# Performance work log

Measured on AMD Instinct MI355X. Metric: run time of the kernel, lower is better.

The kernel has to match this reference:

```python
import jax, jax.numpy as jnp
import numpy as np

N_NODES = 100000
N_EDGES = 3200000  # avg degree 32
D_IN = 256
D_OUT = 256


def setup_inputs() -> dict:
    key = jax.random.key(0)
    k1, k2, k3, k4 = jax.random.split(key, 4)
    x = jax.random.normal(k1, (N_NODES, D_IN), dtype=jnp.float32)
    # nn.Linear(in, out, bias=False): weight shape [out, in]
    W = jax.random.normal(k2, (D_OUT, D_IN), dtype=jnp.float32) / np.sqrt(D_IN).astype(np.float32)
    bias = jnp.zeros((D_OUT,), dtype=jnp.float32)
    rows = jax.random.randint(k3, (N_EDGES,), 0, N_NODES, dtype=jnp.int32)
    cols = jax.random.randint(k4, (N_EDGES,), 0, N_NODES, dtype=jnp.int32)
    return {"x": x, "W": W, "bias": bias, "rows": rows, "cols": cols}


def reference(x, W, bias, rows, cols):
    # aggr == 'planetoid-gcn-residual' branch; dropout p=0 (identity).
    n = x.shape[0]
    h = x @ W.T + bias                                      # [N, D_out]
    # adj_t.sum(dim=-1): per-row degree of binary adjacency
    deg = jax.ops.segment_sum(jnp.ones(rows.shape, x.dtype), rows, num_segments=n)
    norm = jax.lax.rsqrt(1.0 + deg)[:, None]                # [N, 1]
    h = norm * h
    # spmm_add(adj_t, h)[i] = sum_{(i,j) in E} h[j]
    agg = jax.ops.segment_sum(h[cols], rows, num_segments=n)
    h = agg + h
    return norm * h
```

## Files before the change

kernel.cpp:

```cpp
#include <hip/hip_runtime.h>
#include <hip/hip_fp16.h>
#include <stdint.h>


#define THREADS 256

typedef _Float16 half8 __attribute__((ext_vector_type(8)));
typedef float floatx4 __attribute__((ext_vector_type(4)));

__global__ void rank_kernel(const int* __restrict__ rows, int* __restrict__ cnt,
                            int* __restrict__ rank, int E) {
    int e = (blockIdx.x * THREADS + threadIdx.x) * 4;
    if (e + 3 < E) {
        int4 r4 = *(const int4*)(rows + e);
        int4 k;
        k.x = atomicAdd(&cnt[r4.x], 1);
        k.y = atomicAdd(&cnt[r4.y], 1);
        k.z = atomicAdd(&cnt[r4.z], 1);
        k.w = atomicAdd(&cnt[r4.w], 1);
        *(int4*)(rank + e) = k;
    } else {
        for (int i = e; i < E && i < e + 4; ++i)
            rank[i] = atomicAdd(&cnt[rows[i]], 1);
    }
}

__global__ void scanA(const int* __restrict__ cnt, int* __restrict__ rs,
                      int* __restrict__ bsums, int n) {
    __shared__ int s[THREADS];
    int tid  = threadIdx.x;
    int base = blockIdx.x * 1024 + tid * 4;
    int v0 = (base + 0 < n) ? cnt[base + 0] : 0;
    int v1 = (base + 1 < n) ? cnt[base + 1] : 0;
    int v2 = (base + 2 < n) ? cnt[base + 2] : 0;
    int v3 = (base + 3 < n) ? cnt[base + 3] : 0;
    int sum = v0 + v1 + v2 + v3;
    s[tid] = sum;
    __syncthreads();
    for (int off = 1; off < THREADS; off <<= 1) {
        int t = (tid >= off) ? s[tid - off] : 0;
        __syncthreads();
        s[tid] += t;
        __syncthreads();
    }
    int run = s[tid] - sum;
    if (base + 0 < n) rs[base + 0] = run;  run += v0;
    if (base + 1 < n) rs[base + 1] = run;  run += v1;
    if (base + 2 < n) rs[base + 2] = run;  run += v2;
    if (base + 3 < n) rs[base + 3] = run;
    if (tid == THREADS - 1) bsums[blockIdx.x] = s[THREADS - 1];
}

__global__ void scanB(int* __restrict__ bsums, int nb) {
    __shared__ int s[THREADS];
    int tid = threadIdx.x;
    int v = (tid < nb) ? bsums[tid] : 0;
    s[tid] = v;
    __syncthreads();
    for (int off = 1; off < THREADS; off <<= 1) {
        int t = (tid >= off) ? s[tid - off] : 0;
        __syncthreads();
        s[tid] += t;
        __syncthreads();
    }
    if (tid < nb) bsums[tid] = s[tid] - v;
}

__global__ void scanC(int* __restrict__ rs, const int* __restrict__ bsums, int n, int E) {
    int tid  = threadIdx.x;
    int base = blockIdx.x * 1024 + tid * 4;
    int add  = bsums[blockIdx.x];
    if (base + 0 < n) rs[base + 0] += add;
    if (base + 1 < n) rs[base + 1] += add;
    if (base + 2 < n) rs[base + 2] += add;
    if (base + 3 < n) rs[base + 3] += add;
    if (blockIdx.x == 0 && tid == 0) rs[n] = E;
}

__global__ void scatter2(const int* __restrict__ rows, const int* __restrict__ cols,
                         const int* __restrict__ rank, const int* __restrict__ rs,
                         int* __restrict__ csr_col, int E) {
    int e = (blockIdx.x * THREADS + threadIdx.x) * 4;
    if (e + 3 < E) {
        int4 r4 = *(const int4*)(rows + e);
        int4 c4 = *(const int4*)(cols + e);
        int4 k4 = *(const int4*)(rank + e);
        csr_col[rs[r4.x] + k4.x] = c4.x;
        csr_col[rs[r4.y] + k4.y] = c4.y;
        csr_col[rs[r4.z] + k4.z] = c4.z;
        csr_col[rs[r4.w] + k4.w] = c4.w;
    } else {
        for (int i = e; i < E && i < e + 4; ++i)
            csr_col[rs[rows[i]] + rank[i]] = cols[i];
    }
}

__global__ void make_bswz(const float* __restrict__ W, half8* __restrict__ Bswz) {
    int t = blockIdx.x * THREADS + threadIdx.x;
    int n_tile = t >> 9;
    int k_step = (t >> 6) & 7;
    int lane   = t & 63;
    int q = lane >> 4, m16 = lane & 15;
    const float* src = W + (size_t)(n_tile * 16 + m16) * 256 + k_step * 32 + q * 8;
    half8 h;
#pragma unroll
    for (int j = 0; j < 8; j++) h[j] = (_Float16)src[j];
    Bswz[t] = h;
}

__device__ __forceinline__ int As_swz(int b) {
    return b ^ ((((b >> 10) & 7) ^ (((b >> 8) & 1) << 3)) << 4);
}

__global__ __launch_bounds__(THREADS) void gemm_mfma(
    const float* __restrict__ x, const half8* __restrict__ Bswz,
    const float* __restrict__ bias, const int* __restrict__ rs,
    _Float16* __restrict__ h16, int n) {
    __shared__ _Float16 As[4 * 8 * 64 * 8];
    int tid  = threadIdx.x;
    int row0 = blockIdx.x * 64;

#pragma unroll
    for (int i = 0; i < 16; i++) {
        int flat = i * THREADS + tid;
        int r  = flat >> 6;
        int k  = (flat & 63) * 4;
        float4 v;
        if (row0 + r < n) v = *(const float4*)(x + (size_t)(row0 + r) * 256 + k);
        else { v.x = 0.f; v.y = 0.f; v.z = 0.f; v.w = 0.f; }
        int m_sub  = r >> 4;
        int k_step = k >> 5;
        int q      = (k >> 3) & 3;
        int j      = k & 7;
        int lane_w = (r & 15) + (q << 4);
        int entry  = (m_sub * 8 + k_step) * 64 + lane_w;
        union { _Float16 h[4]; uint2 u; } pk;
        pk.h[0] = (_Float16)v.x; pk.h[1] = (_Float16)v.y;
        pk.h[2] = (_Float16)v.z; pk.h[3] = (_Float16)v.w;
        *(uint2*)((char*)As + As_swz(entry * 16 + (j << 1))) = pk.u;
    }
    __syncthreads();

    int w    = tid >> 6;
    int lane = tid & 63;

    floatx4 acc[4][4];
#pragma unroll
    for (int ms = 0; ms < 4; ms++)
#pragma unroll
        for (int nn = 0; nn < 4; nn++) {
            acc[ms][nn][0] = 0.f; acc[ms][nn][1] = 0.f;
            acc[ms][nn][2] = 0.f; acc[ms][nn][3] = 0.f;
        }

    for (int ks = 0; ks < 8; ks++) {
        half8 bfrag[4];
#pragma unroll
        for (int nn = 0; nn < 4; nn++)
            bfrag[nn] = Bswz[((w * 4 + nn) * 8 + ks) * 64 + lane];
        half8 afrag[4];
#pragma unroll
        for (int ms = 0; ms < 4; ms++)
            afrag[ms] = *(const half8*)((char*)As +
                            As_swz(((ms * 8 + ks) * 64 + lane) * 16));
#pragma unroll
        for (int ms = 0; ms < 4; ms++)
#pragma unroll
            for (int nn = 0; nn < 4; nn++)
                acc[ms][nn] = __builtin_amdgcn_mfma_f32_16x16x32_f16(
                    afrag[ms], bfrag[nn], acc[ms][nn], 0, 0, 0);
    }

    int rgrp = lane >> 4;
    int cl   = lane & 15;
#pragma unroll
    for (int ms = 0; ms < 4; ms++) {
        int rbase = row0 + ms * 16 + rgrp * 4;
        float nrm[4];
#pragma unroll
        for (int i = 0; i < 4; i++) {
            int r = rbase + i;
            nrm[i] = (r < n) ? rsqrtf(1.0f + (float)(rs[r + 1] - rs[r])) : 0.f;
        }
#pragma unroll
        for (int nn = 0; nn < 4; nn++) {
            int col = w * 64 + nn * 16 + cl;
            float bb = bias[col];
#pragma unroll
            for (int i = 0; i < 4; i++) {
                int r = rbase + i;
                if (r < n)
                    h16[(size_t)r * 256 + col] =
                        (_Float16)((acc[ms][nn][i] + bb) * nrm[i]);
            }
        }
    }
}

__global__ __launch_bounds__(THREADS) void agg_half(
    const _Float16* __restrict__ h16, const int* __restrict__ csr_col,
    const int* __restrict__ rs, float* __restrict__ out, int n, int halfsel) {
    int row = blockIdx.x * 4 + (threadIdx.x >> 6);
    if (row >= n) return;
    int lane = threadIdx.x & 63;
    int g    = lane >> 4;
    int l16  = lane & 15;
    int off  = halfsel * 128 + l16 * 8;
    const _Float16* hb = h16 + off;

    int s   = rs[row];
    int end = rs[row + 1];

    float acc[8] = {0.f, 0.f, 0.f, 0.f, 0.f, 0.f, 0.f, 0.f};
    if (g == 0) {
        half8 v = *(const half8*)(hb + (size_t)row * 256);
#pragma unroll
        for (int j = 0; j < 8; j++) acc[j] = (float)v[j];
    }

    int e = s + g;
    for (; e + 4 < end; e += 8) {
        int c0 = csr_col[e];
        int c1 = csr_col[e + 4];
        half8 v0 = *(const half8*)(hb + (size_t)c0 * 256);
        half8 v1 = *(const half8*)(hb + (size_t)c1 * 256);
#pragma unroll
        for (int j = 0; j < 8; j++) acc[j] += (float)v0[j] + (float)v1[j];
    }
    for (; e < end; e += 4) {
        int c = csr_col[e];
        half8 v = *(const half8*)(hb + (size_t)c * 256);
#pragma unroll
        for (int j = 0; j < 8; j++) acc[j] += (float)v[j];
    }

#pragma unroll
    for (int j = 0; j < 8; j++) acc[j] += __shfl_down(acc[j], 32);
#pragma unroll
    for (int j = 0; j < 8; j++) acc[j] += __shfl_down(acc[j], 16);

    if (g == 0) {
        float nrm = rsqrtf(1.0f + (float)(end - s));
        float4 o0, o1;
        o0.x = acc[0] * nrm; o0.y = acc[1] * nrm; o0.z = acc[2] * nrm; o0.w = acc[3] * nrm;
        o1.x = acc[4] * nrm; o1.y = acc[5] * nrm; o1.z = acc[6] * nrm; o1.w = acc[7] * nrm;
        float* dst = out + (size_t)row * 256 + off;
        *(float4*)dst       = o0;
        *(float4*)(dst + 4) = o1;
    }
}

extern "C" void kernel_launch(void* const* d_in, const int* in_sizes, int n_in,
                              void* d_out, int out_size, void* d_ws, size_t ws_size,
                              hipStream_t stream) {
    const float* x    = (const float*)d_in[0];
    const float* W    = (const float*)d_in[1];
    const float* bias = (const float*)d_in[2];
    const int*   rows = (const int*)d_in[3];
    const int*   cols = (const int*)d_in[4];

    const int D = 256;
    int n = in_sizes[0] / D;
    int E = in_sizes[3];

    char* p = (char*)d_ws;
    auto alignup = [](size_t v) { return (v + 255) & ~(size_t)255; };
    _Float16* h16 = (_Float16*)p; p += alignup((size_t)n * D * sizeof(_Float16));
    int*   cnt    = (int*)p;    p += alignup((size_t)n * sizeof(int));
    int*   rs     = (int*)p;    p += alignup((size_t)(n + 1) * sizeof(int));
    int*   bsums  = (int*)p;    p += alignup((size_t)1024);
    int*   csr    = (int*)p;    p += alignup((size_t)E * sizeof(int));
    half8* Bswz   = (half8*)p;  p += alignup((size_t)8192 * sizeof(half8));

    int* rank = (int*)h16;

    hipMemsetAsync(cnt, 0, (size_t)n * sizeof(int), stream);

    int e4blocks = ((E + 3) / 4 + THREADS - 1) / THREADS;
    rank_kernel<<<e4blocks, THREADS, 0, stream>>>(rows, cnt, rank, E);

    int nb = (n + 1023) / 1024;
    scanA<<<nb, THREADS, 0, stream>>>(cnt, rs, bsums, n);
    scanB<<<1, THREADS, 0, stream>>>(bsums, nb);
    scanC<<<nb, THREADS, 0, stream>>>(rs, bsums, n, E);

    scatter2<<<e4blocks, THREADS, 0, stream>>>(rows, cols, rank, rs, csr, E);

    make_bswz<<<32, THREADS, 0, stream>>>(W, Bswz);

    int gblocks = (n + 63) / 64;
    gemm_mfma<<<gblocks, THREADS, 0, stream>>>(x, Bswz, bias, rs, h16, n);

    int ablocks = (n + 3) / 4;
    agg_half<<<ablocks, THREADS, 0, stream>>>(h16, csr, rs, (float*)d_out, n, 0);
    agg_half<<<ablocks, THREADS, 0, stream>>>(h16, csr, rs, (float*)d_out, n, 1);
}
```

Before: 666.9 us.

## Build CSR via two-level bucket sort with shared-memory histograms

```diff
diff --git a/kernel.cpp b/kernel.cpp
--- a/kernel.cpp
+++ b/kernel.cpp
@@ -4,36 +4,46 @@
 
 
 #define THREADS 256
+#define MAXBUCK 800
+#define B3_EDGES 16384
 
 typedef _Float16 half8 __attribute__((ext_vector_type(8)));
 typedef float floatx4 __attribute__((ext_vector_type(4)));
 
-__global__ void rank_kernel(const int* __restrict__ rows, int* __restrict__ cnt,
-                            int* __restrict__ rank, int E) {
-    int e = (blockIdx.x * THREADS + threadIdx.x) * 4;
-    if (e + 3 < E) {
-        int4 r4 = *(const int4*)(rows + e);
-        int4 k;
-        k.x = atomicAdd(&cnt[r4.x], 1);
-        k.y = atomicAdd(&cnt[r4.y], 1);
-        k.z = atomicAdd(&cnt[r4.z], 1);
-        k.w = atomicAdd(&cnt[r4.w], 1);
-        *(int4*)(rank + e) = k;
-    } else {
-        for (int i = e; i < E && i < e + 4; ++i)
-            rank[i] = atomicAdd(&cnt[rows[i]], 1);
-    }
-}
-
-__global__ void scanA(const int* __restrict__ cnt, int* __restrict__ rs,
-                      int* __restrict__ bsums, int n) {
+__global__ __launch_bounds__(THREADS) void bucket_count(
+    const int* __restrict__ rows, int* __restrict__ bcnt, int E, int nbuck) {
+    __shared__ int h[MAXBUCK];
+    for (int b = threadIdx.x; b < nbuck; b += THREADS) h[b] = 0;
+    __syncthreads();
+    int nquad  = E >> 2;
+    int stride = gridDim.x * THREADS;
+    for (int q = blockIdx.x * THREADS + threadIdx.x; q < nquad; q += stride) {
+        int4 r = ((const int4*)rows)[q];
+        atomicAdd(&h[r.x >> 7], 1);
+        atomicAdd(&h[r.y >> 7], 1);
+        atomicAdd(&h[r.z >> 7], 1);
+        atomicAdd(&h[r.w >> 7], 1);
+    }
+    if (blockIdx.x == 0)
+        for (int e = (nquad << 2) + threadIdx.x; e < E; e += THREADS)
+            atomicAdd(&h[rows[e] >> 7], 1);
+    __syncthreads();
+    for (int b = threadIdx.x; b < nbuck; b += THREADS) {
+        int v = h[b];
+        if (v) atomicAdd(&bcnt[b], v);
+    }
+}
+
+__global__ __launch_bounds__(THREADS) void bucket_scan(
+    const int* __restrict__ bcnt, int* __restrict__ boff, int* __restrict__ bcur,
+    int nbuck, int E) {
     __shared__ int s[THREADS];
-    int tid  = threadIdx.x;
-    int base = blockIdx.x * 1024 + tid * 4;
-    int v0 = (base + 0 < n) ? cnt[base + 0] : 0;
-    int v1 = (base + 1 < n) ? cnt[base + 1] : 0;
-    int v2 = (base + 2 < n) ? cnt[base + 2] : 0;
-    int v3 = (base + 3 < n) ? cnt[base + 3] : 0;
+    int tid = threadIdx.x;
+    int i0  = tid * 4;
+    int v0 = (i0 + 0 < nbuck) ? bcnt[i0 + 0] : 0;
+    int v1 = (i0 + 1 < nbuck) ? bcnt[i0 + 1] : 0;
+    int v2 = (i0 + 2 < nbuck) ? bcnt[i0 + 2] : 0;
+    int v3 = (i0 + 3 < nbuck) ? bcnt[i0 + 3] : 0;
     int sum = v0 + v1 + v2 + v3;
     s[tid] = sum;
     __syncthreads();
@@ -44,54 +54,75 @@
         __syncthreads();
     }
     int run = s[tid] - sum;
-    if (base + 0 < n) rs[base + 0] = run;  run += v0;
-    if (base + 1 < n) rs[base + 1] = run;  run += v1;
-    if (base + 2 < n) rs[base + 2] = run;  run += v2;
-    if (base + 3 < n) rs[base + 3] = run;
-    if (tid == THREADS - 1) bsums[blockIdx.x] = s[THREADS - 1];
-}
-
-__global__ void scanB(int* __restrict__ bsums, int nb) {
-    __shared__ int s[THREADS];
-    int tid = threadIdx.x;
-    int v = (tid < nb) ? bsums[tid] : 0;
-    s[tid] = v;
-    __syncthreads();
-    for (int off = 1; off < THREADS; off <<= 1) {
-        int t = (tid >= off) ? s[tid - off] : 0;
+    if (i0 + 0 < nbuck) { boff[i0 + 0] = run; bcur[i0 + 0] = run; }  run += v0;
+    if (i0 + 1 < nbuck) { boff[i0 + 1] = run; bcur[i0 + 1] = run; }  run += v1;
+    if (i0 + 2 < nbuck) { boff[i0 + 2] = run; bcur[i0 + 2] = run; }  run += v2;
+    if (i0 + 3 < nbuck) { boff[i0 + 3] = run; bcur[i0 + 3] = run; }
+    if (tid == 0) boff[nbuck] = E;
+}
+
+__global__ __launch_bounds__(THREADS) void bucket_scatter(
+    const int* __restrict__ rows, const int* __restrict__ cols,
+    int* __restrict__ bcur, int2* __restrict__ buf, int E, int nbuck) {
+    __shared__ int h[MAXBUCK];
+    __shared__ int lbase[MAXBUCK];
+    for (int b = threadIdx.x; b < nbuck; b += THREADS) h[b] = 0;
+    __syncthreads();
+    int e0 = blockIdx.x * B3_EDGES;
+    int e1 = e0 + B3_EDGES; if (e1 > E) e1 = E;
+    for (int e = e0 + threadIdx.x; e < e1; e += THREADS)
+        atomicAdd(&h[rows[e] >> 7], 1);
+    __syncthreads();
+    for (int b = threadIdx.x; b < nbuck; b += THREADS) {
+        int v = h[b];
+        lbase[b] = v ? atomicAdd(&bcur[b], v) : 0;
+        h[b] = 0;
+    }
+    __syncthreads();
+    for (int e = e0 + threadIdx.x; e < e1; e += THREADS) {
+        int r = rows[e];
+        int c = cols[e];
+        int b = r >> 7;
+        int p = lbase[b] + atomicAdd(&h[b], 1);
+        buf[p] = make_int2(r, c);
+    }
+}
+
+__global__ __launch_bounds__(THREADS) void csr_finalize(
+    const int2* __restrict__ buf, const int* __restrict__ boff,
+    int* __restrict__ rs, int* __restrict__ csr, int n, int E) {
+    int b = blockIdx.x;
+    __shared__ int h[128];
+    __shared__ int base[128];
+    if (threadIdx.x < 128) h[threadIdx.x] = 0;
+    __syncthreads();
+    int s = boff[b], e = boff[b + 1];
+    for (int i = s + threadIdx.x; i < e; i += THREADS)
+        atomicAdd(&h[buf[i].x & 127], 1);
+    __syncthreads();
+    if (threadIdx.x < 128) base[threadIdx.x] = h[threadIdx.x];
+    __syncthreads();
+    for (int off = 1; off < 128; off <<= 1) {
+        int t = 0;
+        if (threadIdx.x < 128 && threadIdx.x >= off) t = base[threadIdx.x - off];
         __syncthreads();
-        s[tid] += t;
+        if (threadIdx.x < 128) base[threadIdx.x] += t;
         __syncthreads();
     }
-    if (tid < nb) bsums[tid] = s[tid] - v;
-}
-
-__global__ void scanC(int* __restrict__ rs, const int* __restrict__ bsums, int n, int E) {
-    int tid  = threadIdx.x;
-    int base = blockIdx.x * 1024 + tid * 4;
-    int add  = bsums[blockIdx.x];
-    if (base + 0 < n) rs[base + 0] += add;
-    if (base + 1 < n) rs[base + 1] += add;
-    if (base + 2 < n) rs[base + 2] += add;
-    if (base + 3 < n) rs[base + 3] += add;
-    if (blockIdx.x == 0 && tid == 0) rs[n] = E;
-}
-
-__global__ void scatter2(const int* __restrict__ rows, const int* __restrict__ cols,
-                         const int* __restrict__ rank, const int* __restrict__ rs,
-                         int* __restrict__ csr_col, int E) {
-    int e = (blockIdx.x * THREADS + threadIdx.x) * 4;
-    if (e + 3 < E) {
-        int4 r4 = *(const int4*)(rows + e);
-        int4 c4 = *(const int4*)(cols + e);
-        int4 k4 = *(const int4*)(rank + e);
-        csr_col[rs[r4.x] + k4.x] = c4.x;
-        csr_col[rs[r4.y] + k4.y] = c4.y;
-        csr_col[rs[r4.z] + k4.z] = c4.z;
-        csr_col[rs[r4.w] + k4.w] = c4.w;
-    } else {
-        for (int i = e; i < E && i < e + 4; ++i)
-            csr_col[rs[rows[i]] + rank[i]] = cols[i];
+    if (threadIdx.x < 128) {
+        int excl = s + base[threadIdx.x] - h[threadIdx.x];
+        base[threadIdx.x] = excl;
+        int row = (b << 7) + threadIdx.x;
+        if (row < n) rs[row] = excl;
+        h[threadIdx.x] = 0;
+    }
+    if (b == 0 && threadIdx.x == 0) rs[n] = E;
+    __syncthreads();
+    for (int i = s + threadIdx.x; i < e; i += THREADS) {
+        int2 rc = buf[i];
+        int rl = rc.x & 127;
+        int p = base[rl] + atomicAdd(&h[rl], 1);
+        csr[p] = rc.y;
     }
 }
 
@@ -262,29 +293,29 @@
     const int D = 256;
     int n = in_sizes[0] / D;
     int E = in_sizes[3];
+    int nbuck = (n + 127) >> 7;
 
     char* p = (char*)d_ws;
     auto alignup = [](size_t v) { return (v + 255) & ~(size_t)255; };
     _Float16* h16 = (_Float16*)p; p += alignup((size_t)n * D * sizeof(_Float16));
-    int*   cnt    = (int*)p;    p += alignup((size_t)n * sizeof(int));
     int*   rs     = (int*)p;    p += alignup((size_t)(n + 1) * sizeof(int));
-    int*   bsums  = (int*)p;    p += alignup((size_t)1024);
     int*   csr    = (int*)p;    p += alignup((size_t)E * sizeof(int));
     half8* Bswz   = (half8*)p;  p += alignup((size_t)8192 * sizeof(half8));
-
-    int* rank = (int*)h16;
-
-    hipMemsetAsync(cnt, 0, (size_t)n * sizeof(int), stream);
-
-    int e4blocks = ((E + 3) / 4 + THREADS - 1) / THREADS;
-    rank_kernel<<<e4blocks, THREADS, 0, stream>>>(rows, cnt, rank, E);
-
-    int nb = (n + 1023) / 1024;
-    scanA<<<nb, THREADS, 0, stream>>>(cnt, rs, bsums, n);
-    scanB<<<1, THREADS, 0, stream>>>(bsums, nb);
-    scanC<<<nb, THREADS, 0, stream>>>(rs, bsums, n, E);
-
-    scatter2<<<e4blocks, THREADS, 0, stream>>>(rows, cols, rank, rs, csr, E);
+    int*   bcnt   = (int*)p;    p += alignup((size_t)MAXBUCK * sizeof(int));
+    int*   boff   = (int*)p;    p += alignup((size_t)(MAXBUCK + 1) * sizeof(int));
+    int*   bcur   = (int*)p;    p += alignup((size_t)MAXBUCK * sizeof(int));
+
+    int2* buf = (int2*)h16;
+
+    hipMemsetAsync(bcnt, 0, (size_t)nbuck * sizeof(int), stream);
+
+    bucket_count<<<256, THREADS, 0, stream>>>(rows, bcnt, E, nbuck);
+    bucket_scan<<<1, THREADS, 0, stream>>>(bcnt, boff, bcur, nbuck, E);
+
+    int b3blocks = (E + B3_EDGES - 1) / B3_EDGES;
+    bucket_scatter<<<b3blocks, THREADS, 0, stream>>>(rows, cols, bcur, buf, E, nbuck);
+
+    csr_finalize<<<nbuck, THREADS, 0, stream>>>(buf, boff, rs, csr, n, E);
 
     make_bswz<<<32, THREADS, 0, stream>>>(W, Bswz);
 
```

Result: faster. 570.8 us (-14.4%).
